# Optimization experiments

Hardware: AMD Instinct MI355X
Metric: run time of the kernel (lower is better)

The kernel has to match this reference:

```python
import jax, jax.numpy as jnp
import numpy as np

EMBED = 1024
HEADS = 16
HEAD_DIM = EMBED // HEADS
B, L = 4, 2048


def setup_inputs() -> dict:
    key = jax.random.key(0)
    ks = jax.random.split(key, 10)
    s = 1.0 / np.sqrt(EMBED)
    x = jax.random.normal(ks[0], (B, L, EMBED), dtype=jnp.float32)
    mask = jax.random.randint(ks[1], (B, 1, L, L), 0, 2, dtype=jnp.int32)
    Wq = jax.random.normal(ks[2], (EMBED, EMBED), dtype=jnp.float32) * s
    Wk = jax.random.normal(ks[3], (EMBED, EMBED), dtype=jnp.float32) * s
    Wv = jax.random.normal(ks[4], (EMBED, EMBED), dtype=jnp.float32) * s
    Wo = jax.random.normal(ks[5], (EMBED, EMBED), dtype=jnp.float32) * s
    bq = jnp.zeros((EMBED,), jnp.float32)
    bk = jnp.zeros((EMBED,), jnp.float32)
    bv = jnp.zeros((EMBED,), jnp.float32)
    bo = jnp.zeros((EMBED,), jnp.float32)
    return {"x": x, "mask": mask, "Wq": Wq, "bq": bq, "Wk": Wk, "bk": bk,
            "Wv": Wv, "bv": bv, "Wo": Wo, "bo": bo}


def reference(x, mask, Wq, bq, Wk, bk, Wv, bv, Wo, bo):
    n, l, _ = x.shape
    q = (x @ Wq + bq).reshape(n, l, HEADS, HEAD_DIM)
    k = (x @ Wk + bk).reshape(n, l, HEADS, HEAD_DIM)
    v = (x @ Wv + bv).reshape(n, l, HEADS, HEAD_DIM)
    # [n, h, q, k] scores
    energy = jnp.einsum('nqhd,nkhd->nhqk', q, k)
    energy = jnp.where(mask == 0, jnp.float32(-1e20), energy)
    attn = jax.nn.softmax(energy / jnp.sqrt(jnp.float32(HEAD_DIM)), axis=-1)
    out = jnp.einsum('nhqk,nkhd->nqhd', attn, v).reshape(n, l, EMBED)
    return out @ Wo + bo
```

## Files before the change

kernel.cpp:

```cpp
#include <hip/hip_runtime.h>
#include <hip/hip_bf16.h>

#define EMBED 1024
#define HEADS 16
#define HDIM 64
#define BATCH 4
#define SEQ 2048
#define ROWS (BATCH * SEQ)
#define LOG2E 1.4426950408889634f

typedef __attribute__((ext_vector_type(8))) short bf16x8;
typedef __attribute__((ext_vector_type(4))) float f32x4;

#define MFMA16(a, b, c) __builtin_amdgcn_mfma_f32_16x16x32_bf16(a, b, c, 0, 0, 0)

__device__ __forceinline__ unsigned short f2bf(float f) {
    union { float f; unsigned int u; } x; x.f = f;
    unsigned int r = x.u + 0x7fffu + ((x.u >> 16) & 1u);
    return (unsigned short)(r >> 16);
}

__device__ __forceinline__ unsigned int pkbf(float a, float b) {
#if __has_builtin(__builtin_amdgcn_cvt_pk_bf16_f32)
    auto v = __builtin_amdgcn_cvt_pk_bf16_f32(a, b);
    unsigned int u; __builtin_memcpy(&u, &v, 4); return u;
#else
    union { __hip_bfloat162 h; unsigned int u; } c;
    c.h = __float22bfloat162_rn(make_float2(a, b)); return c.u;
#endif
}

__device__ __forceinline__ void gl2lds(const unsigned short* g, unsigned short* l) {
    __builtin_amdgcn_global_load_lds(
        (const __attribute__((address_space(1))) unsigned int*)g,
        (__attribute__((address_space(3))) unsigned int*)l, 16, 0, 0);
}

#define XBLK 8192
#define MBLK 16384
#define WBLK 4096

__global__ __launch_bounds__(256) void prep_kernel(
    const float* __restrict__ x, const int* __restrict__ mask,
    const float* __restrict__ W0, const float* __restrict__ W1,
    const float* __restrict__ W2, const float* __restrict__ W3,
    unsigned short* __restrict__ Xb, unsigned char* __restrict__ m8,
    unsigned short* __restrict__ Wt)
{
    __shared__ float t[32][33];
    const int bid = blockIdx.x;
    if (bid < XBLK) {
        int i = (bid * 256 + threadIdx.x) * 4;
        float4 v = *(const float4*)(x + i);
        uint2 o; o.x = pkbf(v.x, v.y); o.y = pkbf(v.z, v.w);
        *(uint2*)(Xb + i) = o;
    } else if (bid < XBLK + MBLK) {
        int i = ((bid - XBLK) * 256 + threadIdx.x) * 4;
        int4 v = *(const int4*)(mask + i);
        uchar4 o;
        o.x = v.x ? 0xFF : 0; o.y = v.y ? 0xFF : 0;
        o.z = v.z ? 0xFF : 0; o.w = v.w ? 0xFF : 0;
        *(uchar4*)(m8 + i) = o;
    } else {
        int f = bid - XBLK - MBLK;
        int z = f >> 10, rem = f & 1023;
        const float* W = (z == 0) ? W0 : (z == 1) ? W1 : (z == 2) ? W2 : W3;
        unsigned short* o = Wt + (size_t)z * EMBED * EMBED;
        int tx = threadIdx.x & 31, ty = threadIdx.x >> 5;
        int bx = (rem & 31) * 32, by = (rem >> 5) * 32;
#pragma unroll
        for (int r = 0; r < 32; r += 8)
            t[ty + r][tx] = W[(size_t)(by + ty + r) * EMBED + bx + tx];
        __syncthreads();
#pragma unroll
        for (int r = 0; r < 32; r += 8)
            o[(size_t)(bx + ty + r) * EMBED + by + tx] = f2bf(t[tx][ty + r]);
    }
}

__device__ __forceinline__ void gemm_bf16_body(
    const unsigned short* __restrict__ A, const unsigned short* __restrict__ Bt,
    const float* __restrict__ bias,
    float* __restrict__ outF, unsigned short* __restrict__ outB, float scale,
    int vmode)
{
    __shared__ unsigned short As[128][64];
    __shared__ unsigned short Bs[128][64];
    const int tid = threadIdx.x;
    const int lane = tid & 63, wid = tid >> 6;
    const int ln = lane & 15, lg = lane >> 4;
    const int wy = wid >> 1, wx = wid & 1;
    const int m0 = blockIdx.y * 128, n0 = blockIdx.x * 128;
    const int r0 = wid * 32 + (lane >> 3);
    const int scol = (((lane & 7) ^ ((lane >> 3) & 7)) << 3);
    const unsigned short* Ap = A + (size_t)(m0 + r0) * EMBED + scol;
    const unsigned short* Bp = Bt + (size_t)(n0 + r0) * EMBED + scol;
    unsigned short* lA = &As[wid * 32][0];
    unsigned short* lB = &Bs[wid * 32][0];

    f32x4 acc[4][4];
#pragma unroll
    for (int i = 0; i < 4; i++)
#pragma unroll
        for (int j = 0; j < 4; j++) acc[i][j] = (f32x4){0.f, 0.f, 0.f, 0.f};

    for (int k0 = 0; k0 < EMBED; k0 += 64) {
        __syncthreads();
#pragma unroll
        for (int is = 0; is < 4; is++) {
            gl2lds(Ap + k0 + (size_t)(is * 8) * EMBED, lA + is * 8 * 64);
            gl2lds(Bp + k0 + (size_t)(is * 8) * EMBED, lB + is * 8 * 64);
        }
        __syncthreads();
        bf16x8 af[2][4], bfr[2][4];
#pragma unroll
        for (int s = 0; s < 2; s++) {
#pragma unroll
            for (int mi = 0; mi < 4; mi++)
                af[s][mi] = *(const bf16x8*)
                    &As[wy * 64 + mi * 16 + ln][(((lg + 4 * s) ^ (ln & 7)) << 3)];
#pragma unroll
            for (int nj = 0; nj < 4; nj++)
                bfr[s][nj] = *(const bf16x8*)
                    &Bs[wx * 64 + nj * 16 + ln][(((lg + 4 * s) ^ (ln & 7)) << 3)];
        }
#pragma unroll
        for (int s = 0; s < 2; s++)
#pragma unroll
            for (int mi = 0; mi < 4; mi++)
#pragma unroll
                for (int nj = 0; nj < 4; nj++)
                    acc[mi][nj] = MFMA16(af[s][mi], bfr[s][nj], acc[mi][nj]);
    }

#pragma unroll
    for (int mi = 0; mi < 4; mi++) {
#pragma unroll
        for (int nj = 0; nj < 4; nj++) {
            int row = m0 + wy * 64 + mi * 16 + lg * 4;
            int col = n0 + wx * 64 + nj * 16 + ln;
            float bv = bias[col];
            if (vmode) {
                int bb = row >> 11, s = row & (SEQ - 1);
                int hh = col >> 6, dd = col & 63;
                unsigned short* dst = outB +
                    ((size_t)((bb * HEADS + hh) * HDIM + dd)) * SEQ + s;
                uint2 pw;
                pw.x = pkbf(acc[mi][nj][0] + bv, acc[mi][nj][1] + bv);
                pw.y = pkbf(acc[mi][nj][2] + bv, acc[mi][nj][3] + bv);
                *(uint2*)dst = pw;
            } else {
#pragma unroll
                for (int r = 0; r < 4; r++) {
                    float v = (acc[mi][nj][r] + bv) * scale;
                    if (outF) outF[(size_t)(row + r) * EMBED + col] = v;
                    else      outB[(size_t)(row + r) * EMBED + col] = f2bf(v);
                }
            }
        }
    }
}

__global__ __launch_bounds__(256) void qkv_gemm_kernel(
    const unsigned short* __restrict__ Xb, const unsigned short* __restrict__ Wt,
    const float* __restrict__ bq, const float* __restrict__ bk,
    const float* __restrict__ bv,
    unsigned short* __restrict__ Qb, unsigned short* __restrict__ Kb,
    unsigned short* __restrict__ Vt)
{
    int z = blockIdx.z;
    const unsigned short* Bt = Wt + (size_t)z * EMBED * EMBED;
    const float* bias = (z == 0) ? bq : (z == 1) ? bk : bv;
    unsigned short* out = (z == 0) ? Qb : (z == 1) ? Kb : Vt;
    float scale = (z == 0) ? 0.125f * LOG2E : 1.0f;
    gemm_bf16_body(Xb, Bt, bias, nullptr, out, scale, z == 2);
}

__global__ __launch_bounds__(256) void out_gemm_kernel(
    const unsigned short* __restrict__ Ob, const unsigned short* __restrict__ Wto,
    const float* __restrict__ bo, float* __restrict__ out)
{
    gemm_bf16_body(Ob, Wto, bo, out, nullptr, 1.0f, 0);
}

__global__ __launch_bounds__(256) void attn_mfma_kernel(
    const unsigned short* __restrict__ Qb, const unsigned short* __restrict__ Kb,
    const unsigned short* __restrict__ Vt, const unsigned char* __restrict__ mask8,
    unsigned short* __restrict__ Ob)
{
    __shared__ unsigned short Ks[64][64];
    __shared__ unsigned short Vs[64][64];
    __shared__ unsigned short Ps[4][32][64];
    const int tid = threadIdx.x;
    const int lane = tid & 63, wid = tid >> 6;
    const int ln = lane & 15, lg = lane >> 4;
    const int b = blockIdx.z, h = blockIdx.y;
    const int q0 = blockIdx.x * 128 + wid * 32;

    bf16x8 qf[2][2];
#pragma unroll
    for (int mi = 0; mi < 2; mi++)
#pragma unroll
        for (int ks = 0; ks < 2; ks++)
            qf[mi][ks] = *(const bf16x8*)(Qb +
                (size_t)(b * SEQ + q0 + mi * 16 + ln) * EMBED + h * HDIM + ks * 32 + lg * 8);

    bf16x8 ones;
#pragma unroll
    for (int i = 0; i < 8; i++) ones[i] = (short)0x3F80;

    f32x4 o[2][4];
#pragma unroll
    for (int mi = 0; mi < 2; mi++)
#pragma unroll
        for (int dj = 0; dj < 4; dj++) o[mi][dj] = (f32x4){0.f, 0.f, 0.f, 0.f};
    f32x4 lacc[2] = {(f32x4){0.f, 0.f, 0.f, 0.f}, (f32x4){0.f, 0.f, 0.f, 0.f}};

    const int srow = tid >> 3;
    const int scolKV = (((tid & 7) ^ ((tid >> 3) & 7)) << 3);
    const unsigned short* Kp = Kb + (size_t)(b * SEQ + srow) * EMBED + h * HDIM + scolKV;
    const unsigned short* Vp = Vt + (size_t)((b * HEADS + h) * HDIM + srow) * SEQ + scolKV;
    unsigned short* lK = &Ks[srow & ~7][0];
    unsigned short* lV = &Vs[srow & ~7][0];

    const unsigned char* mq0 = mask8 + (size_t)b * SEQ * SEQ + (size_t)(q0 + ln) * SEQ;
    const unsigned char* mq1 = mq0 + (size_t)16 * SEQ;

    const int swk = ((lg ^ (ln & 7)) << 3);

    int pwr[4], prd[2];
#pragma unroll
    for (int nj = 0; nj < 4; nj++)
        pwr[nj] = (((2 * nj + (lg >> 1)) ^ (ln & 7)) << 3) + ((lg & 1) << 2);
#pragma unroll
    for (int ks = 0; ks < 2; ks++)
        prd[ks] = ((4 * ks + lg) ^ (ln & 7)) << 3;
    unsigned short* ps0 = &Ps[wid][ln][0];
    unsigned short* ps1 = &Ps[wid][16 + ln][0];

    for (int kt = 0; kt < SEQ; kt += 64) {
        unsigned int mw[2][4];
#pragma unroll
        for (int mi = 0; mi < 2; mi++) {
            const unsigned char* mq = (mi ? mq1 : mq0) + kt;
#pragma unroll
            for (int nj = 0; nj < 4; nj++)
                mw[mi][nj] = *(const unsigned int*)(mq + nj * 16 + lg * 4);
        }

        __syncthreads();
        gl2lds(Kp + (size_t)kt * EMBED, lK);
        gl2lds(Kp + (size_t)(kt + 32) * EMBED, lK + 32 * 64);
        gl2lds(Vp + kt, lV);
        gl2lds(Vp + (size_t)32 * SEQ + kt, lV + 32 * 64);
        __syncthreads();

        f32x4 S[2][4];
#pragma unroll
        for (int nj = 0; nj < 4; nj++) {
            bf16x8 k0 = *(const bf16x8*)&Ks[nj * 16 + ln][swk];
            bf16x8 k1 = *(const bf16x8*)&Ks[nj * 16 + ln][swk ^ 32];
#pragma unroll
            for (int mi = 0; mi < 2; mi++) {
                f32x4 t2 = (f32x4){0.f, 0.f, 0.f, 0.f};
                t2 = MFMA16(k0, qf[mi][0], t2);
                t2 = MFMA16(k1, qf[mi][1], t2);
                S[mi][nj] = t2;
            }
        }

#pragma unroll
        for (int mi = 0; mi < 2; mi++) {
            unsigned short* psb = mi ? ps1 : ps0;
#pragma unroll
            for (int nj = 0; nj < 4; nj++) {
                float p0 = __builtin_amdgcn_exp2f(S[mi][nj][0]);
                float p1 = __builtin_amdgcn_exp2f(S[mi][nj][1]);
                float p2 = __builtin_amdgcn_exp2f(S[mi][nj][2]);
                float p3 = __builtin_amdgcn_exp2f(S[mi][nj][3]);
                unsigned int m = mw[mi][nj];
                unsigned int d0 = __builtin_amdgcn_perm(0u, m, 0x01010000u);
                unsigned int d1 = __builtin_amdgcn_perm(0u, m, 0x03030202u);
                uint2 pw;
                pw.x = pkbf(p0, p1) & d0;
                pw.y = pkbf(p2, p3) & d1;
                *(uint2*)(psb + pwr[nj]) = pw;
            }
        }

#pragma unroll
        for (int ks = 0; ks < 2; ks++) {
            bf16x8 p0 = *(const bf16x8*)(ps0 + prd[ks]);
            bf16x8 p1 = *(const bf16x8*)(ps1 + prd[ks]);
            lacc[0] = MFMA16(p0, ones, lacc[0]);
            lacc[1] = MFMA16(p1, ones, lacc[1]);
#pragma unroll
            for (int dj = 0; dj < 4; dj++) {
                bf16x8 vf = *(const bf16x8*)&Vs[dj * 16 + ln][swk ^ (ks << 5)];
                o[0][dj] = MFMA16(p0, vf, o[0][dj]);
                o[1][dj] = MFMA16(p1, vf, o[1][dj]);
            }
        }
    }

#pragma unroll
    for (int mi = 0; mi < 2; mi++) {
        float l0 = 1.0f / lacc[mi][0];
        float l1 = 1.0f / lacc[mi][1];
        float l2 = 1.0f / lacc[mi][2];
        float l3 = 1.0f / lacc[mi][3];
#pragma unroll
        for (int dj = 0; dj < 4; dj++) {
            unsigned short* op = Ob + (size_t)(b * SEQ + q0 + mi * 16 + lg * 4) * EMBED
                                    + h * HDIM + dj * 16 + ln;
            op[0]         = f2bf(o[mi][dj][0] * l0);
            op[EMBED]     = f2bf(o[mi][dj][1] * l1);
            op[2 * EMBED] = f2bf(o[mi][dj][2] * l2);
            op[3 * EMBED] = f2bf(o[mi][dj][3] * l3);
        }
    }
}

extern "C" void kernel_launch(void* const* d_in, const int* in_sizes, int n_in,
                              void* d_out, int out_size, void* d_ws, size_t ws_size,
                              hipStream_t stream)
{
    const float* x  = (const float*)d_in[0];
    const int* mask = (const int*)d_in[1];
    const float* Wq = (const float*)d_in[2];
    const float* bq = (const float*)d_in[3];
    const float* Wk = (const float*)d_in[4];
    const float* bk = (const float*)d_in[5];
    const float* Wv = (const float*)d_in[6];
    const float* bv = (const float*)d_in[7];
    const float* Wo = (const float*)d_in[8];
    const float* bo = (const float*)d_in[9];
    float* outp = (float*)d_out;

    char* ws = (char*)d_ws;
    unsigned short* Wt = (unsigned short*)(ws);
    unsigned char*  m8 = (unsigned char*)(ws + ((size_t)8 << 20));
    unsigned short* Xb = (unsigned short*)(ws + ((size_t)24 << 20));
    unsigned short* Ob = Xb;
    unsigned short* Qb = (unsigned short*)(ws + ((size_t)40 << 20));
    unsigned short* Kb = (unsigned short*)(ws + ((size_t)56 << 20));
    unsigned short* Vt = (unsigned short*)(ws + ((size_t)72 << 20));

    prep_kernel<<<XBLK + MBLK + WBLK, 256, 0, stream>>>(
        x, mask, Wq, Wk, Wv, Wo, Xb, m8, Wt);
    qkv_gemm_kernel<<<dim3(EMBED / 128, ROWS / 128, 3), 256, 0, stream>>>(
        Xb, Wt, bq, bk, bv, Qb, Kb, Vt);
    attn_mfma_kernel<<<dim3(SEQ / 128, HEADS, BATCH), 256, 0, stream>>>(
        Qb, Kb, Vt, m8, Ob);
    out_gemm_kernel<<<dim3(EMBED / 128, ROWS / 128), 256, 0, stream>>>(
        Ob, Wt + (size_t)3 * EMBED * EMBED, bo, outp);
}
```

Measured before the change: 397.9 us.

## Double-buffer LDS tiles in GEMM and attention with 32-wide K steps

Both the projection GEMM and the attention kernel now split their K dimension into 32-wide tiles held in two LDS buffers. Each iteration issues the global-to-LDS loads for the next tile (and, in attention, the next mask words) before computing on the current one, so each loop iteration needs one barrier instead of two. The swizzle patterns are rewritten for the narrower 32-column tiles. The aim is to overlap memory latency with MFMA work, at the cost of more loop iterations and a harmless redundant wrap-around prefetch on the last step. Correctness depends on the async LDS loads being complete by the barrier.

```diff
diff --git a/kernel.cpp b/kernel.cpp
--- a/kernel.cpp
+++ b/kernel.cpp
@@ -84,19 +84,20 @@
     float* __restrict__ outF, unsigned short* __restrict__ outB, float scale,
     int vmode)
 {
-    __shared__ unsigned short As[128][64];
-    __shared__ unsigned short Bs[128][64];
+    __shared__ unsigned short As[2][128][32];
+    __shared__ unsigned short Bs[2][128][32];
     const int tid = threadIdx.x;
     const int lane = tid & 63, wid = tid >> 6;
     const int ln = lane & 15, lg = lane >> 4;
     const int wy = wid >> 1, wx = wid & 1;
     const int m0 = blockIdx.y * 128, n0 = blockIdx.x * 128;
-    const int r0 = wid * 32 + (lane >> 3);
-    const int scol = (((lane & 7) ^ ((lane >> 3) & 7)) << 3);
-    const unsigned short* Ap = A + (size_t)(m0 + r0) * EMBED + scol;
-    const unsigned short* Bp = Bt + (size_t)(n0 + r0) * EMBED + scol;
-    unsigned short* lA = &As[wid * 32][0];
-    unsigned short* lB = &Bs[wid * 32][0];
+    const int r0 = wid * 32 + (lane >> 2);
+    const int logc = (((lane & 3) ^ ((lane >> 2) & 3) ^ ((lane >> 4) & 3)) << 3);
+    const unsigned short* Ap = A + (size_t)(m0 + r0) * EMBED + logc;
+    const unsigned short* Bp = Bt + (size_t)(n0 + r0) * EMBED + logc;
+    unsigned short* lA[2] = {&As[0][wid * 32][0], &As[1][wid * 32][0]};
+    unsigned short* lB[2] = {&Bs[0][wid * 32][0], &Bs[1][wid * 32][0]};
+    const int swg = ((lg ^ (ln & 3) ^ (ln >> 2)) << 3);
 
     f32x4 acc[4][4];
 #pragma unroll
@@ -104,33 +105,34 @@
 #pragma unroll
         for (int j = 0; j < 4; j++) acc[i][j] = (f32x4){0.f, 0.f, 0.f, 0.f};
 
-    for (int k0 = 0; k0 < EMBED; k0 += 64) {
+    gl2lds(Ap, lA[0]);
+    gl2lds(Ap + (size_t)16 * EMBED, lA[0] + 16 * 32);
+    gl2lds(Bp, lB[0]);
+    gl2lds(Bp + (size_t)16 * EMBED, lB[0] + 16 * 32);
+
+    const int NK = EMBED / 32;
+    for (int t = 0; t < NK; t++) {
+        const int cur = t & 1;
         __syncthreads();
-#pragma unroll
-        for (int is = 0; is < 4; is++) {
-            gl2lds(Ap + k0 + (size_t)(is * 8) * EMBED, lA + is * 8 * 64);
-            gl2lds(Bp + k0 + (size_t)(is * 8) * EMBED, lB + is * 8 * 64);
-        }
-        __syncthreads();
-        bf16x8 af[2][4], bfr[2][4];
-#pragma unroll
-        for (int s = 0; s < 2; s++) {
-#pragma unroll
-            for (int mi = 0; mi < 4; mi++)
-                af[s][mi] = *(const bf16x8*)
-                    &As[wy * 64 + mi * 16 + ln][(((lg + 4 * s) ^ (ln & 7)) << 3)];
+        {
+            const int kn = ((t + 1) & (NK - 1)) * 32;
+            gl2lds(Ap + kn, lA[cur ^ 1]);
+            gl2lds(Ap + kn + (size_t)16 * EMBED, lA[cur ^ 1] + 16 * 32);
+            gl2lds(Bp + kn, lB[cur ^ 1]);
+            gl2lds(Bp + kn + (size_t)16 * EMBED, lB[cur ^ 1] + 16 * 32);
+        }
+        bf16x8 af[4], bfr[4];
+#pragma unroll
+        for (int mi = 0; mi < 4; mi++)
+            af[mi] = *(const bf16x8*)&As[cur][wy * 64 + mi * 16 + ln][swg];
+#pragma unroll
+        for (int nj = 0; nj < 4; nj++)
+            bfr[nj] = *(const bf16x8*)&Bs[cur][wx * 64 + nj * 16 + ln][swg];
+#pragma unroll
+        for (int mi = 0; mi < 4; mi++)
 #pragma unroll
             for (int nj = 0; nj < 4; nj++)
-                bfr[s][nj] = *(const bf16x8*)
-                    &Bs[wx * 64 + nj * 16 + ln][(((lg + 4 * s) ^ (ln & 7)) << 3)];
-        }
-#pragma unroll
-        for (int s = 0; s < 2; s++)
-#pragma unroll
-            for (int mi = 0; mi < 4; mi++)
-#pragma unroll
-                for (int nj = 0; nj < 4; nj++)
-                    acc[mi][nj] = MFMA16(af[s][mi], bfr[s][nj], acc[mi][nj]);
+                acc[mi][nj] = MFMA16(af[mi], bfr[nj], acc[mi][nj]);
     }
 
 #pragma unroll
@@ -188,9 +190,9 @@
     const unsigned short* __restrict__ Vt, const unsigned char* __restrict__ mask8,
     unsigned short* __restrict__ Ob)
 {
-    __shared__ unsigned short Ks[64][64];
-    __shared__ unsigned short Vs[64][64];
-    __shared__ unsigned short Ps[4][32][64];
+    __shared__ unsigned short Ks[2][32][64];
+    __shared__ unsigned short Vs[2][64][32];
+    __shared__ unsigned short Ps[4][32][32];
     const int tid = threadIdx.x;
     const int lane = tid & 63, wid = tid >> 6;
     const int ln = lane & 15, lg = lane >> 4;
@@ -216,50 +218,56 @@
         for (int dj = 0; dj < 4; dj++) o[mi][dj] = (f32x4){0.f, 0.f, 0.f, 0.f};
     f32x4 lacc[2] = {(f32x4){0.f, 0.f, 0.f, 0.f}, (f32x4){0.f, 0.f, 0.f, 0.f}};
 
-    const int srow = tid >> 3;
-    const int scolKV = (((tid & 7) ^ ((tid >> 3) & 7)) << 3);
-    const unsigned short* Kp = Kb + (size_t)(b * SEQ + srow) * EMBED + h * HDIM + scolKV;
-    const unsigned short* Vp = Vt + (size_t)((b * HEADS + h) * HDIM + srow) * SEQ + scolKV;
-    unsigned short* lK = &Ks[srow & ~7][0];
-    unsigned short* lV = &Vs[srow & ~7][0];
+    const int krow = wid * 8 + (lane >> 3);
+    const int kc = (((lane & 7) ^ ((lane >> 3) & 7)) << 3);
+    const unsigned short* Kp = Kb + (size_t)(b * SEQ + krow) * EMBED + h * HDIM + kc;
+    const int vrow = wid * 16 + (lane >> 2);
+    const int vc = (((lane & 3) ^ ((lane >> 2) & 3) ^ ((lane >> 4) & 3)) << 3);
+    const unsigned short* Vp = Vt + (size_t)((b * HEADS + h) * HDIM + vrow) * SEQ + vc;
+    unsigned short* lK[2] = {&Ks[0][wid * 8][0], &Ks[1][wid * 8][0]};
+    unsigned short* lV[2] = {&Vs[0][wid * 16][0], &Vs[1][wid * 16][0]};
 
     const unsigned char* mq0 = mask8 + (size_t)b * SEQ * SEQ + (size_t)(q0 + ln) * SEQ;
     const unsigned char* mq1 = mq0 + (size_t)16 * SEQ;
 
     const int swk = ((lg ^ (ln & 7)) << 3);
-
-    int pwr[4], prd[2];
-#pragma unroll
-    for (int nj = 0; nj < 4; nj++)
-        pwr[nj] = (((2 * nj + (lg >> 1)) ^ (ln & 7)) << 3) + ((lg & 1) << 2);
-#pragma unroll
-    for (int ks = 0; ks < 2; ks++)
-        prd[ks] = ((4 * ks + lg) ^ (ln & 7)) << 3;
+    const int swv = ((lg ^ (ln & 3) ^ (ln >> 2)) << 3);
+    int pwr[2];
+#pragma unroll
+    for (int nj = 0; nj < 2; nj++)
+        pwr[nj] = (((2 * nj + (lg >> 1)) ^ (ln & 3) ^ (ln >> 2)) << 3) + ((lg & 1) << 2);
     unsigned short* ps0 = &Ps[wid][ln][0];
     unsigned short* ps1 = &Ps[wid][16 + ln][0];
 
-    for (int kt = 0; kt < SEQ; kt += 64) {
-        unsigned int mw[2][4];
-#pragma unroll
-        for (int mi = 0; mi < 2; mi++) {
-            const unsigned char* mq = (mi ? mq1 : mq0) + kt;
-#pragma unroll
-            for (int nj = 0; nj < 4; nj++)
-                mw[mi][nj] = *(const unsigned int*)(mq + nj * 16 + lg * 4);
-        }
-
+    unsigned int mwc[2][2];
+#pragma unroll
+    for (int mi = 0; mi < 2; mi++)
+#pragma unroll
+        for (int nj = 0; nj < 2; nj++)
+            mwc[mi][nj] = *(const unsigned int*)((mi ? mq1 : mq0) + nj * 16 + lg * 4);
+    gl2lds(Kp, lK[0]);
+    gl2lds(Vp, lV[0]);
+
+    const int NT = SEQ / 32;
+    for (int t = 0; t < NT; t++) {
+        const int cur = t & 1;
         __syncthreads();
-        gl2lds(Kp + (size_t)kt * EMBED, lK);
-        gl2lds(Kp + (size_t)(kt + 32) * EMBED, lK + 32 * 64);
-        gl2lds(Vp + kt, lV);
-        gl2lds(Vp + (size_t)32 * SEQ + kt, lV + 32 * 64);
-        __syncthreads();
-
-        f32x4 S[2][4];
-#pragma unroll
-        for (int nj = 0; nj < 4; nj++) {
-            bf16x8 k0 = *(const bf16x8*)&Ks[nj * 16 + ln][swk];
-            bf16x8 k1 = *(const bf16x8*)&Ks[nj * 16 + ln][swk ^ 32];
+
+        const int ktn = ((t + 1) & (NT - 1)) * 32;
+        unsigned int mwn[2][2];
+#pragma unroll
+        for (int mi = 0; mi < 2; mi++)
+#pragma unroll
+            for (int nj = 0; nj < 2; nj++)
+                mwn[mi][nj] = *(const unsigned int*)((mi ? mq1 : mq0) + ktn + nj * 16 + lg * 4);
+        gl2lds(Kp + (size_t)ktn * EMBED, lK[cur ^ 1]);
+        gl2lds(Vp + ktn, lV[cur ^ 1]);
+
+        f32x4 S[2][2];
+#pragma unroll
+        for (int nj = 0; nj < 2; nj++) {
+            bf16x8 k0 = *(const bf16x8*)&Ks[cur][nj * 16 + ln][swk];
+            bf16x8 k1 = *(const bf16x8*)&Ks[cur][nj * 16 + ln][swk ^ 32];
 #pragma unroll
             for (int mi = 0; mi < 2; mi++) {
                 f32x4 t2 = (f32x4){0.f, 0.f, 0.f, 0.f};
@@ -273,12 +281,12 @@
         for (int mi = 0; mi < 2; mi++) {
             unsigned short* psb = mi ? ps1 : ps0;
 #pragma unroll
-            for (int nj = 0; nj < 4; nj++) {
+            for (int nj = 0; nj < 2; nj++) {
                 float p0 = __builtin_amdgcn_exp2f(S[mi][nj][0]);
                 float p1 = __builtin_amdgcn_exp2f(S[mi][nj][1]);
                 float p2 = __builtin_amdgcn_exp2f(S[mi][nj][2]);
                 float p3 = __builtin_amdgcn_exp2f(S[mi][nj][3]);
-                unsigned int m = mw[mi][nj];
+                unsigned int m = mwc[mi][nj];
                 unsigned int d0 = __builtin_amdgcn_perm(0u, m, 0x01010000u);
                 unsigned int d1 = __builtin_amdgcn_perm(0u, m, 0x03030202u);
                 uint2 pw;
@@ -289,18 +297,20 @@
         }
 
 #pragma unroll
-        for (int ks = 0; ks < 2; ks++) {
-            bf16x8 p0 = *(const bf16x8*)(ps0 + prd[ks]);
-            bf16x8 p1 = *(const bf16x8*)(ps1 + prd[ks]);
-            lacc[0] = MFMA16(p0, ones, lacc[0]);
-            lacc[1] = MFMA16(p1, ones, lacc[1]);
+        for (int mi = 0; mi < 2; mi++) {
+            bf16x8 p = *(const bf16x8*)((mi ? ps1 : ps0) + swv);
+            lacc[mi] = MFMA16(p, ones, lacc[mi]);
 #pragma unroll
             for (int dj = 0; dj < 4; dj++) {
-                bf16x8 vf = *(const bf16x8*)&Vs[dj * 16 + ln][swk ^ (ks << 5)];
-                o[0][dj] = MFMA16(p0, vf, o[0][dj]);
-                o[1][dj] = MFMA16(p1, vf, o[1][dj]);
+                bf16x8 vf = *(const bf16x8*)&Vs[cur][dj * 16 + ln][swv];
+                o[mi][dj] = MFMA16(p, vf, o[mi][dj]);
             }
         }
+
+#pragma unroll
+        for (int mi = 0; mi < 2; mi++)
+#pragma unroll
+            for (int nj = 0; nj < 2; nj++) mwc[mi][nj] = mwn[mi][nj];
     }
 
 #pragma unroll
```

New measurement: 445.1 us. 11.9% more time.
